# Performance work log

Hardware: AMD Instinct MI355X
Metric: run time of the kernel (lower is better)

The kernel has to match this reference:

```python
import jax, jax.numpy as jnp
import numpy as np

T, H, NH, NKV, HD, E, K, I = 1024, 2048, 16, 4, 128, 16, 2, 768
EPS = 1e-6
THETA = 10000.0


def setup_inputs() -> dict:
    key = jax.random.key(0)
    ks = jax.random.split(key, 8)
    s = 0.02
    return {
        "hidden_states": jax.random.normal(ks[0], (T, H), jnp.float32),
        "positions": jnp.arange(T, dtype=jnp.int32),
        "w_norm1": jnp.ones((H,), jnp.float32),
        "w_norm2": jnp.ones((H,), jnp.float32),
        "w_qkv": jax.random.normal(ks[1], (H, (NH + 2 * NKV) * HD), jnp.float32) * s,
        "w_qnorm": jnp.ones((HD,), jnp.float32),
        "w_knorm": jnp.ones((HD,), jnp.float32),
        "w_o": jax.random.normal(ks[2], (NH * HD, H), jnp.float32) * s,
        "w_router": jax.random.normal(ks[3], (H, E), jnp.float32) * s,
        "w_gate": jax.random.normal(ks[4], (E, H, I), jnp.float32) * s,
        "w_up": jax.random.normal(ks[5], (E, H, I), jnp.float32) * s,
        "w_down": jax.random.normal(ks[6], (E, I, H), jnp.float32) * s,
    }


def rmsnorm(x, w):
    return x * jax.lax.rsqrt(jnp.mean(x * x, axis=-1, keepdims=True) + EPS) * w


def apply_rope(x, positions):
    # NEOX-style rotary, full head_dim. x: [T, n_heads, HD]
    half = HD // 2
    inv_freq = 1.0 / (THETA ** (jnp.arange(half, dtype=jnp.float32) / half))
    ang = positions.astype(jnp.float32)[:, None] * inv_freq  # [T, half]
    cos = jnp.cos(ang)[:, None, :]
    sin = jnp.sin(ang)[:, None, :]
    x1, x2 = x[..., :half], x[..., half:]
    return jnp.concatenate([x1 * cos - x2 * sin, x2 * cos + x1 * sin], axis=-1)


def reference(hidden_states, positions, w_norm1, w_norm2, w_qkv, w_qnorm, w_knorm,
              w_o, w_router, w_gate, w_up, w_down):
    # prepare_attn: residual = x; h = input_layernorm(x)
    residual = hidden_states
    h = rmsnorm(hidden_states, w_norm1)

    # --- attention (bidirectional, GQA, per-head q/k RMSNorm + RoPE) ---
    qkv = h @ w_qkv
    q, k, v = jnp.split(qkv, [NH * HD, NH * HD + NKV * HD], axis=-1)
    q = rmsnorm(q.reshape(T, NH, HD), w_qnorm)
    k = rmsnorm(k.reshape(T, NKV, HD), w_knorm)
    v = v.reshape(T, NKV, HD)
    q = apply_rope(q, positions)
    k = apply_rope(k, positions)
    rep = NH // NKV
    kf = jnp.repeat(k, rep, axis=1)  # [T, NH, HD]
    vf = jnp.repeat(v, rep, axis=1)
    scores = jnp.einsum('tnd,snd->nts', q, kf) * (HD ** -0.5)  # [NH, T, T]
    p = jax.nn.softmax(scores, axis=-1)
    ctx = jnp.einsum('nts,snd->tnd', p, vf).reshape(T, NH * HD)
    attn_out = ctx @ w_o

    # prepare_mlp: residual = residual + attn_out; h = post_attention_layernorm(residual)
    residual = residual + attn_out
    h = rmsnorm(residual, w_norm2)

    # --- sparse MoE: softmax router, top-k renormalize, SwiGLU experts ---
    logits = h @ w_router
    probs = jax.nn.softmax(logits, axis=-1)
    topw, topi = jax.lax.top_k(probs, K)
    topw = topw / jnp.sum(topw, axis=-1, keepdims=True)
    gates = jnp.zeros((T, E), h.dtype).at[jnp.arange(T)[:, None], topi].set(topw)
    g = jnp.einsum('th,ehi->eti', h, w_gate)
    u = jnp.einsum('th,ehi->eti', h, w_up)
    y = jnp.einsum('eti,eih->eth', jax.nn.silu(g) * u, w_down)
    moe_out = jnp.einsum('eth,te->th', y, gates)

    return moe_out, residual
```

## Files before the change

### kernel.cpp

```cpp
#include <hip/hip_runtime.h>

#define T_    1024
#define H_    2048
#define NH_   16
#define NKV_  4
#define HD_   128
#define E_    16
#define I_    768
#define QKVN  3072

typedef __attribute__((ext_vector_type(8))) short  short8;
typedef __attribute__((ext_vector_type(4))) float  f32x4;
typedef unsigned short u16;

#define LDP 40

__device__ inline u16 f2bf(float f) {
  unsigned u = __builtin_bit_cast(unsigned, f);
  return (u16)((u + 0x7fffu + ((u >> 16) & 1u)) >> 16);
}
__device__ inline float bf2f(u16 h) {
  unsigned u = ((unsigned)h) << 16;
  return __builtin_bit_cast(float, u);
}

__device__ inline float blk_sum(float v, float* lds) {
#pragma unroll
  for (int o = 32; o; o >>= 1) v += __shfl_down(v, o);
  int w = threadIdx.x >> 6;
  __syncthreads();
  if ((threadIdx.x & 63) == 0) lds[w] = v;
  __syncthreads();
  float s = lds[0];
  int nw = blockDim.x >> 6;
  for (int i = 1; i < nw; ++i) s += lds[i];
  return s;
}
__device__ inline float blk_max(float v, float* lds) {
#pragma unroll
  for (int o = 32; o; o >>= 1) v = fmaxf(v, __shfl_down(v, o));
  int w = threadIdx.x >> 6;
  __syncthreads();
  if ((threadIdx.x & 63) == 0) lds[w] = v;
  __syncthreads();
  float s = lds[0];
  int nw = blockDim.x >> 6;
  for (int i = 1; i < nw; ++i) s = fmaxf(s, lds[i]);
  return s;
}


struct AU4 { uint4 v; };
struct BU2 { uint2 v; };
struct F4  { float v[4]; };

__device__ inline void wrS(u16* lds, const AU4& r) {
  *(uint4*)(lds + (threadIdx.x >> 2) * LDP + (threadIdx.x & 3) * 8) = r.v;
}
__device__ inline void wrS(u16* lds, const BU2& r) {
  *(uint2*)(lds + (threadIdx.x >> 3) * LDP + (threadIdx.x & 7) * 4) = r.v;
}
__device__ inline void wrS(u16* lds, const F4& r) {
  int n = threadIdx.x & 63, kh = (threadIdx.x >> 6) * 4;
  uint2 w;
  w.x = (unsigned)f2bf(r.v[0]) | ((unsigned)f2bf(r.v[1]) << 16);
  w.y = (unsigned)f2bf(r.v[2]) | ((unsigned)f2bf(r.v[3]) << 16);
  *(uint2*)(lds + n * LDP + kh) = w;
}

__device__ inline void mma2(const u16* As, const u16* Bs, f32x4 acc[2][2]) {
  const int lane = threadIdx.x & 63, wv = threadIdx.x >> 6;
  const int wr = wv >> 1, wc = wv & 1;
  const int kk = (lane >> 4) * 8, rr = lane & 15;
  short8 aF[2], bF[2];
#pragma unroll
  for (int m = 0; m < 2; ++m)
    aF[m] = *(const short8*)(As + (wr * 32 + m * 16 + rr) * LDP + kk);
#pragma unroll
  for (int n = 0; n < 2; ++n)
    bF[n] = *(const short8*)(Bs + (wc * 32 + n * 16 + rr) * LDP + kk);
#pragma unroll
  for (int m = 0; m < 2; ++m)
#pragma unroll
    for (int n = 0; n < 2; ++n)
      acc[m][n] = __builtin_amdgcn_mfma_f32_16x16x32_bf16(aF[m], bF[n], acc[m][n], 0, 0, 0);
}

#define ZERO_ACC(acc) do { \
  _Pragma("unroll") for (int m_ = 0; m_ < 2; ++m_) \
  _Pragma("unroll") for (int n_ = 0; n_ < 2; ++n_) acc[m_][n_] = (f32x4){0.f,0.f,0.f,0.f}; \
} while (0)

#define EPI_ROW(m, r)  (((threadIdx.x >> 6) >> 1) * 32 + (m)*16 + (((threadIdx.x&63) >> 4) * 4) + (r))
#define EPI_COL(n)     ((((threadIdx.x >> 6) & 1) * 32) + (n)*16 + ((threadIdx.x&63) & 15))

template<int NT, class AT, class BT, class LA, class LB>
__device__ inline void pipe2(LA la, LB lb, u16* A0, u16* B0, u16* A1, u16* B1,
                             f32x4 acc[2][2]) {
  AT a0, a1; BT b0, b1;
  la(a0, 0); lb(b0, 0);
  la(a1, 1); lb(b1, 1);
  wrS(A0, a0); wrS(B0, b0);
  if (NT > 2) { la(a0, 2); lb(b0, 2); }
#pragma unroll 1
  for (int kt = 0; kt < NT; kt += 2) {
    __syncthreads();
    wrS(A1, a1); wrS(B1, b1);
    if (kt + 3 < NT) { la(a1, kt + 3); lb(b1, kt + 3); }
    mma2(A0, B0, acc);
    __syncthreads();
    if (kt + 2 < NT) { wrS(A0, a0); wrS(B0, b0); }
    if (kt + 4 < NT) { la(a0, kt + 4); lb(b0, kt + 4); }
    mma2(A1, B1, acc);
  }
}


__global__ __launch_bounds__(256) void k_rms1(const float* x, const float* w, u16* out) {
  __shared__ float lds[4];
  int t = blockIdx.x, tid = threadIdx.x;
  float v[8]; float ss = 0.f;
#pragma unroll
  for (int i = 0; i < 8; ++i) { v[i] = x[(size_t)t * H_ + tid + 256 * i]; ss += v[i] * v[i]; }
  ss = blk_sum(ss, lds);
  float inv = rsqrtf(ss * (1.f / H_) + 1e-6f);
#pragma unroll
  for (int i = 0; i < 8; ++i)
    out[(size_t)t * H_ + tid + 256 * i] = f2bf(v[i] * inv * w[tid + 256 * i]);
}

__global__ __launch_bounds__(256) void k_rms2(const float* x, const float* w,
                                              float* outf, u16* outb) {
  __shared__ float lds[4];
  int t = blockIdx.x, tid = threadIdx.x;
  float v[8]; float ss = 0.f;
#pragma unroll
  for (int i = 0; i < 8; ++i) { v[i] = x[(size_t)t * H_ + tid + 256 * i]; ss += v[i] * v[i]; }
  ss = blk_sum(ss, lds);
  float inv = rsqrtf(ss * (1.f / H_) + 1e-6f);
#pragma unroll
  for (int i = 0; i < 8; ++i) {
    float r = v[i] * inv * w[tid + 256 * i];
    outf[(size_t)t * H_ + tid + 256 * i] = r;
    outb[(size_t)t * H_ + tid + 256 * i] = f2bf(r);
  }
}

__global__ __launch_bounds__(512) void k_qkv(const u16* h1, const float* wqkv, float* qkv) {
  __shared__ __align__(16) u16 A0[128 * LDP], B0[64 * LDP], A1[128 * LDP], B1[64 * LDP];
  int bn = blockIdx.x, bm = blockIdx.y;
  f32x4 acc[2][2]; ZERO_ACC(acc);
  auto la = [&](AU4& r, int kt) {
    r.v = *(const uint4*)(h1 + (size_t)(bm * 128 + (threadIdx.x >> 2)) * H_ + kt * 32 + (threadIdx.x & 3) * 8);
  };
  auto lb = [&](F4& r, int kt) {
    int n = threadIdx.x & 63, kh = (threadIdx.x >> 6) * 4;
    const float* src = wqkv + (size_t)(kt * 32 + kh) * QKVN + bn * 64 + n;
#pragma unroll
    for (int j = 0; j < 4; ++j) r.v[j] = src[(size_t)j * QKVN];
  };
  pipe2<H_ / 32, AU4, F4>(la, lb, A0, B0, A1, B1, acc);
#pragma unroll
  for (int m = 0; m < 2; ++m)
#pragma unroll
    for (int n = 0; n < 2; ++n) {
      f32x4 a = acc[m][n];
#pragma unroll
      for (int r = 0; r < 4; ++r)
        qkv[(size_t)(bm * 128 + EPI_ROW(m, r)) * QKVN + bn * 64 + EPI_COL(n)] = a[r];
    }
}

__global__ __launch_bounds__(256) void k_qkrope(const float* qkv, const int* pos,
                                                const float* wq, const float* wk,
                                                u16* q, u16* kk, u16* vT) {
  __shared__ float cs[64], sn[64];
  int t = blockIdx.x, tid = threadIdx.x, lane = tid & 63, w = tid >> 6;
  if (tid < 64) {
    float fr = expf(-((float)tid / 64.f) * 9.210340371976184f);
    float ang = (float)pos[t] * fr;
    float s_, c_; sincosf(ang, &s_, &c_);
    cs[tid] = c_; sn[tid] = s_;
  }
  __syncthreads();
  const float* row = qkv + (size_t)t * QKVN;
  for (int h = w; h < NH_; h += 4) {
    float x1 = row[h * 128 + lane], x2 = row[h * 128 + 64 + lane];
    float ss = x1 * x1 + x2 * x2;
#pragma unroll
    for (int o = 32; o; o >>= 1) ss += __shfl_down(ss, o);
    ss = __shfl(ss, 0);
    float inv = rsqrtf(ss * (1.f / HD_) + 1e-6f);
    float n1 = x1 * inv * wq[lane], n2 = x2 * inv * wq[64 + lane];
    float o1 = n1 * cs[lane] - n2 * sn[lane];
    float o2 = n2 * cs[lane] + n1 * sn[lane];
    q[(size_t)t * (NH_ * HD_) + h * 128 + lane] = f2bf(o1);
    q[(size_t)t * (NH_ * HD_) + h * 128 + 64 + lane] = f2bf(o2);
  }
  if (w < NKV_) {
    int h = w;
    float x1 = row[2048 + h * 128 + lane], x2 = row[2048 + h * 128 + 64 + lane];
    float ss = x1 * x1 + x2 * x2;
#pragma unroll
    for (int o = 32; o; o >>= 1) ss += __shfl_down(ss, o);
    ss = __shfl(ss, 0);
    float inv = rsqrtf(ss * (1.f / HD_) + 1e-6f);
    float n1 = x1 * inv * wk[lane], n2 = x2 * inv * wk[64 + lane];
    float o1 = n1 * cs[lane] - n2 * sn[lane];
    float o2 = n2 * cs[lane] + n1 * sn[lane];
    kk[((size_t)h * T_ + t) * HD_ + lane] = f2bf(o1);
    kk[((size_t)h * T_ + t) * HD_ + 64 + lane] = f2bf(o2);
    float v1 = row[2560 + h * 128 + lane], v2 = row[2560 + h * 128 + 64 + lane];
    vT[((size_t)(h * 128 + lane)) * T_ + t] = f2bf(v1);
    vT[((size_t)(h * 128 + 64 + lane)) * T_ + t] = f2bf(v2);
  }
}

__global__ __launch_bounds__(512) void k_scores(const u16* q, const u16* kb, u16* S) {
  __shared__ __align__(16) u16 A0[128 * LDP], B0[64 * LDP], A1[128 * LDP], B1[64 * LDP];
  int h = blockIdx.x, sn = blockIdx.y, qm = blockIdx.z;
  const u16* Aq = q + h * 128;
  const u16* Bk = kb + (size_t)(h >> 2) * T_ * HD_;
  f32x4 acc[2][2]; ZERO_ACC(acc);
  auto la = [&](AU4& r, int kt) {
    r.v = *(const uint4*)(Aq + (size_t)(qm * 128 + (threadIdx.x >> 2)) * (NH_ * HD_) + kt * 32 + (threadIdx.x & 3) * 8);
  };
  auto lb = [&](BU2& r, int kt) {
    r.v = *(const uint2*)(Bk + (size_t)(sn * 64 + (threadIdx.x >> 3)) * HD_ + kt * 32 + (threadIdx.x & 7) * 4);
  };
  pipe2<HD_ / 32, AU4, BU2>(la, lb, A0, B0, A1, B1, acc);
  const float scale = 0.08838834764831845f;
#pragma unroll
  for (int m = 0; m < 2; ++m)
#pragma unroll
    for (int n = 0; n < 2; ++n) {
      f32x4 a = acc[m][n];
#pragma unroll
      for (int r = 0; r < 4; ++r)
        S[((size_t)h * T_ + qm * 128 + EPI_ROW(m, r)) * T_ + sn * 64 + EPI_COL(n)] =
            f2bf(a[r] * scale);
    }
}

__global__ __launch_bounds__(256) void k_softmax(u16* S) {
  __shared__ float lds[4];
  int t = blockIdx.x, h = blockIdx.y, tid = threadIdx.x;
  u16* rowp = S + ((size_t)h * T_ + t) * T_;
  float x[4];
#pragma unroll
  for (int i = 0; i < 4; ++i) x[i] = bf2f(rowp[tid + 256 * i]);
  float m = fmaxf(fmaxf(x[0], x[1]), fmaxf(x[2], x[3]));
  m = blk_max(m, lds);
  float s = 0.f;
#pragma unroll
  for (int i = 0; i < 4; ++i) { x[i] = __expf(x[i] - m); s += x[i]; }
  s = blk_sum(s, lds);
  float inv = 1.f / s;
#pragma unroll
  for (int i = 0; i < 4; ++i) rowp[tid + 256 * i] = f2bf(x[i] * inv);
}

__global__ __launch_bounds__(512) void k_pv(const u16* P, const u16* vT, u16* ctx) {
  __shared__ __align__(16) u16 A0[128 * LDP], B0[64 * LDP], A1[128 * LDP], B1[64 * LDP];
  int h = blockIdx.x, qm = blockIdx.y, nb = blockIdx.z;
  const u16* Ap = P + (size_t)h * T_ * T_;
  const u16* Bv = vT + (size_t)(h >> 2) * HD_ * T_ + (size_t)nb * 64 * T_;
  f32x4 acc[2][2]; ZERO_ACC(acc);
  auto la = [&](AU4& r, int kt) {
    r.v = *(const uint4*)(Ap + (size_t)(qm * 128 + (threadIdx.x >> 2)) * T_ + kt * 32 + (threadIdx.x & 3) * 8);
  };
  auto lb = [&](BU2& r, int kt) {
    r.v = *(const uint2*)(Bv + (size_t)(threadIdx.x >> 3) * T_ + kt * 32 + (threadIdx.x & 7) * 4);
  };
  pipe2<T_ / 32, AU4, BU2>(la, lb, A0, B0, A1, B1, acc);
#pragma unroll
  for (int m = 0; m < 2; ++m)
#pragma unroll
    for (int n = 0; n < 2; ++n) {
      f32x4 a = acc[m][n];
#pragma unroll
      for (int r = 0; r < 4; ++r)
        ctx[(size_t)(qm * 128 + EPI_ROW(m, r)) * (NH_ * HD_) + h * 128 + nb * 64 + EPI_COL(n)] =
            f2bf(a[r]);
    }
}

__global__ __launch_bounds__(512) void k_wo(const u16* ctx, const float* wo,
                                            const float* hs, float* resid) {
  __shared__ __align__(16) u16 A0[128 * LDP], B0[64 * LDP], A1[128 * LDP], B1[64 * LDP];
  int bn = blockIdx.x, bm = blockIdx.y;
  f32x4 acc[2][2]; ZERO_ACC(acc);
  auto la = [&](AU4& r, int kt) {
    r.v = *(const uint4*)(ctx + (size_t)(bm * 128 + (threadIdx.x >> 2)) * H_ + kt * 32 + (threadIdx.x & 3) * 8);
  };
  auto lb = [&](F4& r, int kt) {
    int n = threadIdx.x & 63, kh = (threadIdx.x >> 6) * 4;
    const float* src = wo + (size_t)(kt * 32 + kh) * H_ + bn * 64 + n;
#pragma unroll
    for (int j = 0; j < 4; ++j) r.v[j] = src[(size_t)j * H_];
  };
  pipe2<H_ / 32, AU4, F4>(la, lb, A0, B0, A1, B1, acc);
#pragma unroll
  for (int m = 0; m < 2; ++m)
#pragma unroll
    for (int n = 0; n < 2; ++n) {
      f32x4 a = acc[m][n];
#pragma unroll
      for (int r = 0; r < 4; ++r) {
        size_t idx = (size_t)(bm * 128 + EPI_ROW(m, r)) * H_ + bn * 64 + EPI_COL(n);
        resid[idx] = a[r] + hs[idx];
      }
    }
}

__global__ __launch_bounds__(256) void k_router(const float* h2f, const float* wr_,
                                                int* topi, float* topw, int* cnt) {
  __shared__ float xs[H_];
  __shared__ float red[4][16];
  __shared__ float lg[16];
  int t = blockIdx.x, tid = threadIdx.x;
#pragma unroll
  for (int i = 0; i < 8; ++i) xs[tid + 256 * i] = h2f[(size_t)t * H_ + tid + 256 * i];
  __syncthreads();
  int e = tid & 15, p = tid >> 4;
  float s = 0.f;
  int b0 = p * 128;
  for (int i = 0; i < 128; ++i) s += xs[b0 + i] * wr_[(size_t)(b0 + i) * E_ + e];
  s += __shfl_down(s, 32);
  s += __shfl_down(s, 16);
  int lane = tid & 63, w = tid >> 6;
  if (lane < 16) red[w][lane] = s;
  __syncthreads();
  if (tid < 16) lg[tid] = red[0][tid] + red[1][tid] + red[2][tid] + red[3][tid];
  __syncthreads();
  if (tid == 0) {
    float l1 = -1e30f; int e1 = 0;
    for (int i = 0; i < E_; ++i) if (lg[i] > l1) { l1 = lg[i]; e1 = i; }
    float l2 = -1e30f; int e2 = 0;
    for (int i = 0; i < E_; ++i) if (i != e1 && lg[i] > l2) { l2 = lg[i]; e2 = i; }
    float d = __expf(l2 - l1);
    float w1 = 1.f / (1.f + d), w2 = d / (1.f + d);
    topi[2 * t] = e1; topi[2 * t + 1] = e2;
    topw[2 * t] = w1; topw[2 * t + 1] = w2;
    atomicAdd(&cnt[e1], 1);
    atomicAdd(&cnt[e2], 1);
  }
}

__global__ void k_scan(const int* cnt, int* basearr) {
  if (threadIdx.x == 0) {
    int b = 0;
    for (int e = 0; e < E_; ++e) { basearr[e] = b; b += cnt[e]; }
    basearr[E_] = b;
  }
}

__global__ __launch_bounds__(256) void k_assign(const int* topi, const float* topw,
                                                const int* basearr, int* posc,
                                                int* tok, float* wslot) {
  int t = blockIdx.x * 256 + threadIdx.x;
  if (t < T_) {
#pragma unroll
    for (int j = 0; j < 2; ++j) {
      int e = topi[2 * t + j];
      int p = atomicAdd(&posc[e], 1);
      int s = basearr[e] + p;
      tok[s] = t;
      wslot[s] = topw[2 * t + j];
    }
  }
}

__global__ __launch_bounds__(512) void k_gateup(const u16* h2b,
                                                const float* wg, const float* wu,
                                                const int* cnt, const int* basearr, const int* tok,
                                                u16* act) {
  __shared__ __align__(16) u16 A0[128 * LDP], B0[64 * LDP], A1[128 * LDP], B1[64 * LDP];
  __shared__ int gat_s[128];
  int e = blockIdx.x;
  int c = cnt[e];
  int mt = blockIdx.z;
  if (mt * 128 >= c) return;
  int basee = basearr[e];
  int gmax = c - mt * 128;
  int n0 = blockIdx.y * 32;
  int tid = threadIdx.x;
  if (tid < 128) {
    int r = mt * 128 + tid;
    gat_s[tid] = (r < c) ? tok[basee + r] : tok[basee];
  }
  __syncthreads();
  const float* Bg = wg + (size_t)e * H_ * I_;
  const float* Bu = wu + (size_t)e * H_ * I_;
  f32x4 acc[2][2]; ZERO_ACC(acc);
  auto la = [&](AU4& r, int kt) {
    r.v = *(const uint4*)(h2b + (size_t)gat_s[threadIdx.x >> 2] * H_ + kt * 32 + (threadIdx.x & 3) * 8);
  };
  auto lb = [&](F4& r, int kt) {
    int cidx = threadIdx.x & 63, kh = (threadIdx.x >> 6) * 4;
    int fn = cidx >> 4;
    const float* base = (fn & 1) ? Bu : Bg;
    int col = n0 + (fn >> 1) * 16 + (cidx & 15);
    const float* src = base + (size_t)(kt * 32 + kh) * I_ + col;
#pragma unroll
    for (int j = 0; j < 4; ++j) r.v[j] = src[(size_t)j * I_];
  };
  pipe2<H_ / 32, AU4, F4>(la, lb, A0, B0, A1, B1, acc);
  int slot0 = basee + mt * 128;
  int col = n0 + ((threadIdx.x >> 6) & 1) * 16 + ((threadIdx.x & 63) & 15);
#pragma unroll
  for (int m = 0; m < 2; ++m) {
#pragma unroll
    for (int r = 0; r < 4; ++r) {
      int row = EPI_ROW(m, r);
      if (row >= gmax) continue;
      float g = acc[m][0][r], u = acc[m][1][r];
      float sg = g / (1.f + __expf(-g));
      act[(size_t)(slot0 + row) * I_ + col] = f2bf(sg * u);
    }
  }
}

__global__ __launch_bounds__(512) void k_down(const u16* act, const float* wd,
                                              const int* cnt, const int* basearr,
                                              const int* tok, const float* wslot,
                                              float* moe) {
  __shared__ __align__(16) u16 A0[128 * LDP], B0[64 * LDP], A1[128 * LDP], B1[64 * LDP];
  int e = blockIdx.y;
  int c = cnt[e];
  int mt = blockIdx.z;
  if (mt * 128 >= c) return;
  int basee = basearr[e];
  int gmax = c - mt * 128;
  int slot0 = basee + mt * 128;
  int n0 = blockIdx.x * 64;
  const u16* Ap = act + (size_t)slot0 * I_;
  const float* Bp = wd + (size_t)e * I_ * H_;
  f32x4 acc[2][2]; ZERO_ACC(acc);
  auto la = [&](AU4& r, int kt) {
    r.v = *(const uint4*)(Ap + (size_t)(threadIdx.x >> 2) * I_ + kt * 32 + (threadIdx.x & 3) * 8);
  };
  auto lb = [&](F4& r, int kt) {
    int n = threadIdx.x & 63, kh = (threadIdx.x >> 6) * 4;
    const float* src = Bp + (size_t)(kt * 32 + kh) * H_ + n0 + n;
#pragma unroll
    for (int j = 0; j < 4; ++j) r.v[j] = src[(size_t)j * H_];
  };
  pipe2<I_ / 32, AU4, F4>(la, lb, A0, B0, A1, B1, acc);
#pragma unroll
  for (int m = 0; m < 2; ++m)
#pragma unroll
    for (int n = 0; n < 2; ++n) {
      f32x4 a = acc[m][n];
#pragma unroll
      for (int r = 0; r < 4; ++r) {
        int row = EPI_ROW(m, r);
        if (row >= gmax) continue;
        int col = EPI_COL(n);
        int slot = slot0 + row;
        float wgt = wslot[slot];
        int tk = tok[slot];
        atomicAdd(&moe[(size_t)tk * H_ + n0 + col], a[r] * wgt);
      }
    }
}

extern "C" void kernel_launch(void* const* d_in, const int* in_sizes, int n_in,
                              void* d_out, int out_size, void* d_ws, size_t ws_size,
                              hipStream_t stream) {
  const float* hs    = (const float*)d_in[0];
  const int*   pos   = (const int*)d_in[1];
  const float* wn1   = (const float*)d_in[2];
  const float* wn2   = (const float*)d_in[3];
  const float* wqkv  = (const float*)d_in[4];
  const float* wqn   = (const float*)d_in[5];
  const float* wkn   = (const float*)d_in[6];
  const float* wo    = (const float*)d_in[7];
  const float* wrt   = (const float*)d_in[8];
  const float* wg    = (const float*)d_in[9];
  const float* wu    = (const float*)d_in[10];
  const float* wd    = (const float*)d_in[11];
  float* out = (float*)d_out;
  float* moe_out = out;
  float* resid   = out + (size_t)T_ * H_;

  char* ws = (char*)d_ws;
  size_t off = 0;
  auto alloc = [&](size_t bytes) { size_t r = off; off = (off + bytes + 255) & ~(size_t)255; return r; };
  u16*   h1   = (u16*)  (ws + alloc((size_t)T_ * H_ * 2));
  float* qkv  = (float*)(ws + alloc((size_t)T_ * QKVN * 4));
  u16*   q    = (u16*)  (ws + alloc((size_t)T_ * NH_ * HD_ * 2));
  u16*   kb   = (u16*)  (ws + alloc((size_t)NKV_ * T_ * HD_ * 2));
  u16*   vT   = (u16*)  (ws + alloc((size_t)NKV_ * HD_ * T_ * 2));
  u16*   S    = (u16*)  (ws + alloc((size_t)NH_ * T_ * T_ * 2));
  u16*   ctx  = (u16*)  (ws + alloc((size_t)T_ * NH_ * HD_ * 2));
  float* h2f  = (float*)(ws + alloc((size_t)T_ * H_ * 4));
  u16*   h2b  = (u16*)  (ws + alloc((size_t)T_ * H_ * 2));
  u16*   act  = (u16*)  (ws + alloc((size_t)(2 * T_ + 256) * I_ * 2));
  int*   topi = (int*)  (ws + alloc((size_t)T_ * 2 * 4));
  float* topw = (float*)(ws + alloc((size_t)T_ * 2 * 4));
  int*   cnt  = (int*)  (ws + alloc(32 * 4));
  int*   posc = cnt + 16;
  int*   base = (int*)  (ws + alloc(32 * 4));
  int*   tok  = (int*)  (ws + alloc((size_t)(2 * T_ + 128) * 4));
  float* wsl  = (float*)(ws + alloc((size_t)(2 * T_ + 128) * 4));
  (void)ws_size; (void)in_sizes; (void)n_in; (void)out_size;

  hipMemsetAsync(moe_out, 0, (size_t)T_ * H_ * 4, stream);
  hipMemsetAsync(cnt, 0, 32 * 4, stream);

  k_rms1<<<T_, 256, 0, stream>>>(hs, wn1, h1);
  k_qkv<<<dim3(QKVN / 64, T_ / 128), 512, 0, stream>>>(h1, wqkv, qkv);
  k_qkrope<<<T_, 256, 0, stream>>>(qkv, pos, wqn, wkn, q, kb, vT);
  k_scores<<<dim3(NH_, T_ / 64, T_ / 128), 512, 0, stream>>>(q, kb, S);
  k_softmax<<<dim3(T_, NH_), 256, 0, stream>>>(S);
  k_pv<<<dim3(NH_, T_ / 128, HD_ / 64), 512, 0, stream>>>(S, vT, ctx);
  k_wo<<<dim3(H_ / 64, T_ / 128), 512, 0, stream>>>(ctx, wo, hs, resid);
  k_rms2<<<T_, 256, 0, stream>>>(resid, wn2, h2f, h2b);
  k_router<<<T_, 256, 0, stream>>>(h2f, wrt, topi, topw, cnt);
  k_scan<<<1, 64, 0, stream>>>(cnt, base);
  k_assign<<<4, 256, 0, stream>>>(topi, topw, base, posc, tok, wsl);
  k_gateup<<<dim3(E_, I_ / 32, T_ / 128), 512, 0, stream>>>(h2b, wg, wu, cnt, base, tok, act);
  k_down<<<dim3(H_ / 64, E_, T_ / 128), 512, 0, stream>>>(act, wd, cnt, base, tok, wsl, moe_out);
}
```

Measured before the change: 341.5 us.

## Load bf16 GEMM operands directly into LDS via global_load_lds

Replaces the register-staged loads of bf16 operand tiles (A everywhere, plus B in the scores and PV kernels) with the global_load_lds builtin, so data goes straight from global memory into shared memory. A tiles use an unpadded stride of 32 so they match the wave-contiguous layout the instruction writes. Two pipeline variants are added: one for bf16 A with fp32 B still converted in registers, and one fully direct for bf16×bf16. This removes VGPR staging and LDS store instructions, but the unpadded A layout may cause LDS bank conflicts on MFMA fragment reads. The direct loads also depend on __syncthreads being enough to order them, with no explicit vmcnt wait.

```diff
diff --git a/kernel.cpp b/kernel.cpp
--- a/kernel.cpp
+++ b/kernel.cpp
@@ -13,7 +13,8 @@
 typedef __attribute__((ext_vector_type(4))) float  f32x4;
 typedef unsigned short u16;
 
-#define LDP 40
+#define LDPA 32
+#define LDPB 40
 
 __device__ inline u16 f2bf(float f) {
   unsigned u = __builtin_bit_cast(unsigned, f);
@@ -22,6 +23,12 @@
 __device__ inline float bf2f(u16 h) {
   unsigned u = ((unsigned)h) << 16;
   return __builtin_bit_cast(float, u);
+}
+
+__device__ inline void gll16(const u16* g, u16* l) {
+  __builtin_amdgcn_global_load_lds(
+      (const __attribute__((address_space(1))) void*)g,
+      (__attribute__((address_space(3))) void*)l, 16, 0, 0);
 }
 
 __device__ inline float blk_sum(float v, float* lds) {
@@ -50,24 +57,17 @@
 }
 
 
-struct AU4 { uint4 v; };
-struct BU2 { uint2 v; };
-struct F4  { float v[4]; };
-
-__device__ inline void wrS(u16* lds, const AU4& r) {
-  *(uint4*)(lds + (threadIdx.x >> 2) * LDP + (threadIdx.x & 3) * 8) = r.v;
-}
-__device__ inline void wrS(u16* lds, const BU2& r) {
-  *(uint2*)(lds + (threadIdx.x >> 3) * LDP + (threadIdx.x & 7) * 4) = r.v;
-}
+struct F4 { float v[4]; };
+
 __device__ inline void wrS(u16* lds, const F4& r) {
   int n = threadIdx.x & 63, kh = (threadIdx.x >> 6) * 4;
   uint2 w;
   w.x = (unsigned)f2bf(r.v[0]) | ((unsigned)f2bf(r.v[1]) << 16);
   w.y = (unsigned)f2bf(r.v[2]) | ((unsigned)f2bf(r.v[3]) << 16);
-  *(uint2*)(lds + n * LDP + kh) = w;
-}
-
+  *(uint2*)(lds + n * LDPB + kh) = w;
+}
+
+template<int SA, int SB>
 __device__ inline void mma2(const u16* As, const u16* Bs, f32x4 acc[2][2]) {
   const int lane = threadIdx.x & 63, wv = threadIdx.x >> 6;
   const int wr = wv >> 1, wc = wv & 1;
@@ -75,10 +75,10 @@
   short8 aF[2], bF[2];
 #pragma unroll
   for (int m = 0; m < 2; ++m)
-    aF[m] = *(const short8*)(As + (wr * 32 + m * 16 + rr) * LDP + kk);
+    aF[m] = *(const short8*)(As + (wr * 32 + m * 16 + rr) * SA + kk);
 #pragma unroll
   for (int n = 0; n < 2; ++n)
-    bF[n] = *(const short8*)(Bs + (wc * 32 + n * 16 + rr) * LDP + kk);
+    bF[n] = *(const short8*)(Bs + (wc * 32 + n * 16 + rr) * SB + kk);
 #pragma unroll
   for (int m = 0; m < 2; ++m)
 #pragma unroll
@@ -94,24 +94,40 @@
 #define EPI_ROW(m, r)  (((threadIdx.x >> 6) >> 1) * 32 + (m)*16 + (((threadIdx.x&63) >> 4) * 4) + (r))
 #define EPI_COL(n)     ((((threadIdx.x >> 6) & 1) * 32) + (n)*16 + ((threadIdx.x&63) & 15))
 
-template<int NT, class AT, class BT, class LA, class LB>
-__device__ inline void pipe2(LA la, LB lb, u16* A0, u16* B0, u16* A1, u16* B1,
-                             f32x4 acc[2][2]) {
-  AT a0, a1; BT b0, b1;
-  la(a0, 0); lb(b0, 0);
-  la(a1, 1); lb(b1, 1);
-  wrS(A0, a0); wrS(B0, b0);
-  if (NT > 2) { la(a0, 2); lb(b0, 2); }
+template<int NT, class GA, class LB>
+__device__ inline void pipeGF(GA ga, LB lb, u16* A0, u16* B0, u16* A1, u16* B1,
+                              f32x4 acc[2][2]) {
+  F4 b0, b1;
+  ga(A0, 0);
+  lb(b0, 0); lb(b1, 1);
+  wrS(B0, b0);
+  if (NT > 2) lb(b0, 2);
 #pragma unroll 1
   for (int kt = 0; kt < NT; kt += 2) {
     __syncthreads();
-    wrS(A1, a1); wrS(B1, b1);
-    if (kt + 3 < NT) { la(a1, kt + 3); lb(b1, kt + 3); }
-    mma2(A0, B0, acc);
+    ga(A1, kt + 1);
+    wrS(B1, b1);
+    if (kt + 3 < NT) lb(b1, kt + 3);
+    mma2<LDPA, LDPB>(A0, B0, acc);
     __syncthreads();
-    if (kt + 2 < NT) { wrS(A0, a0); wrS(B0, b0); }
-    if (kt + 4 < NT) { la(a0, kt + 4); lb(b0, kt + 4); }
-    mma2(A1, B1, acc);
+    if (kt + 2 < NT) { ga(A0, kt + 2); wrS(B0, b0); }
+    if (kt + 4 < NT) lb(b0, kt + 4);
+    mma2<LDPA, LDPB>(A1, B1, acc);
+  }
+}
+
+template<int NT, class GA, class GB>
+__device__ inline void pipeGG(GA ga, GB gb, u16* A0, u16* B0, u16* A1, u16* B1,
+                              f32x4 acc[2][2]) {
+  ga(A0, 0); gb(B0, 0);
+#pragma unroll 1
+  for (int kt = 0; kt < NT; kt += 2) {
+    __syncthreads();
+    ga(A1, kt + 1); gb(B1, kt + 1);
+    mma2<LDPA, LDPA>(A0, B0, acc);
+    __syncthreads();
+    if (kt + 2 < NT) { ga(A0, kt + 2); gb(B0, kt + 2); }
+    mma2<LDPA, LDPA>(A1, B1, acc);
   }
 }
 
@@ -147,11 +163,13 @@
 }
 
 __global__ __launch_bounds__(512) void k_qkv(const u16* h1, const float* wqkv, float* qkv) {
-  __shared__ __align__(16) u16 A0[128 * LDP], B0[64 * LDP], A1[128 * LDP], B1[64 * LDP];
+  __shared__ __align__(16) u16 A0[128 * LDPA], A1[128 * LDPA];
+  __shared__ __align__(16) u16 B0[64 * LDPB], B1[64 * LDPB];
   int bn = blockIdx.x, bm = blockIdx.y;
   f32x4 acc[2][2]; ZERO_ACC(acc);
-  auto la = [&](AU4& r, int kt) {
-    r.v = *(const uint4*)(h1 + (size_t)(bm * 128 + (threadIdx.x >> 2)) * H_ + kt * 32 + (threadIdx.x & 3) * 8);
+  auto ga = [&](u16* As, int kt) {
+    gll16(h1 + (size_t)(bm * 128 + (threadIdx.x >> 2)) * H_ + kt * 32 + (threadIdx.x & 3) * 8,
+          As + (threadIdx.x & 448) * 8);
   };
   auto lb = [&](F4& r, int kt) {
     int n = threadIdx.x & 63, kh = (threadIdx.x >> 6) * 4;
@@ -159,7 +177,7 @@
 #pragma unroll
     for (int j = 0; j < 4; ++j) r.v[j] = src[(size_t)j * QKVN];
   };
-  pipe2<H_ / 32, AU4, F4>(la, lb, A0, B0, A1, B1, acc);
+  pipeGF<H_ / 32>(ga, lb, A0, B0, A1, B1, acc);
 #pragma unroll
   for (int m = 0; m < 2; ++m)
 #pragma unroll
@@ -217,18 +235,22 @@
 }
 
 __global__ __launch_bounds__(512) void k_scores(const u16* q, const u16* kb, u16* S) {
-  __shared__ __align__(16) u16 A0[128 * LDP], B0[64 * LDP], A1[128 * LDP], B1[64 * LDP];
+  __shared__ __align__(16) u16 A0[128 * LDPA], A1[128 * LDPA];
+  __shared__ __align__(16) u16 B0[64 * LDPA], B1[64 * LDPA];
   int h = blockIdx.x, sn = blockIdx.y, qm = blockIdx.z;
   const u16* Aq = q + h * 128;
   const u16* Bk = kb + (size_t)(h >> 2) * T_ * HD_;
   f32x4 acc[2][2]; ZERO_ACC(acc);
-  auto la = [&](AU4& r, int kt) {
-    r.v = *(const uint4*)(Aq + (size_t)(qm * 128 + (threadIdx.x >> 2)) * (NH_ * HD_) + kt * 32 + (threadIdx.x & 3) * 8);
-  };
-  auto lb = [&](BU2& r, int kt) {
-    r.v = *(const uint2*)(Bk + (size_t)(sn * 64 + (threadIdx.x >> 3)) * HD_ + kt * 32 + (threadIdx.x & 7) * 4);
-  };
-  pipe2<HD_ / 32, AU4, BU2>(la, lb, A0, B0, A1, B1, acc);
+  auto ga = [&](u16* As, int kt) {
+    gll16(Aq + (size_t)(qm * 128 + (threadIdx.x >> 2)) * (NH_ * HD_) + kt * 32 + (threadIdx.x & 3) * 8,
+          As + (threadIdx.x & 448) * 8);
+  };
+  auto gb = [&](u16* Bs, int kt) {
+    if (threadIdx.x < 256)
+      gll16(Bk + (size_t)(sn * 64 + (threadIdx.x >> 2)) * HD_ + kt * 32 + (threadIdx.x & 3) * 8,
+            Bs + (threadIdx.x & 192) * 8);
+  };
+  pipeGG<HD_ / 32>(ga, gb, A0, B0, A1, B1, acc);
   const float scale = 0.08838834764831845f;
 #pragma unroll
   for (int m = 0; m < 2; ++m)
@@ -261,18 +283,22 @@
 }
 
 __global__ __launch_bounds__(512) void k_pv(const u16* P, const u16* vT, u16* ctx) {
-  __shared__ __align__(16) u16 A0[128 * LDP], B0[64 * LDP], A1[128 * LDP], B1[64 * LDP];
+  __shared__ __align__(16) u16 A0[128 * LDPA], A1[128 * LDPA];
+  __shared__ __align__(16) u16 B0[64 * LDPA], B1[64 * LDPA];
   int h = blockIdx.x, qm = blockIdx.y, nb = blockIdx.z;
   const u16* Ap = P + (size_t)h * T_ * T_;
   const u16* Bv = vT + (size_t)(h >> 2) * HD_ * T_ + (size_t)nb * 64 * T_;
   f32x4 acc[2][2]; ZERO_ACC(acc);
-  auto la = [&](AU4& r, int kt) {
-    r.v = *(const uint4*)(Ap + (size_t)(qm * 128 + (threadIdx.x >> 2)) * T_ + kt * 32 + (threadIdx.x & 3) * 8);
-  };
-  auto lb = [&](BU2& r, int kt) {
-    r.v = *(const uint2*)(Bv + (size_t)(threadIdx.x >> 3) * T_ + kt * 32 + (threadIdx.x & 7) * 4);
-  };
-  pipe2<T_ / 32, AU4, BU2>(la, lb, A0, B0, A1, B1, acc);
+  auto ga = [&](u16* As, int kt) {
+    gll16(Ap + (size_t)(qm * 128 + (threadIdx.x >> 2)) * T_ + kt * 32 + (threadIdx.x & 3) * 8,
+          As + (threadIdx.x & 448) * 8);
+  };
+  auto gb = [&](u16* Bs, int kt) {
+    if (threadIdx.x < 256)
+      gll16(Bv + (size_t)(threadIdx.x >> 2) * T_ + kt * 32 + (threadIdx.x & 3) * 8,
+            Bs + (threadIdx.x & 192) * 8);
+  };
+  pipeGG<T_ / 32>(ga, gb, A0, B0, A1, B1, acc);
 #pragma unroll
   for (int m = 0; m < 2; ++m)
 #pragma unroll
@@ -287,11 +313,13 @@
 
 __global__ __launch_bounds__(512) void k_wo(const u16* ctx, const float* wo,
                                             const float* hs, float* resid) {
-  __shared__ __align__(16) u16 A0[128 * LDP], B0[64 * LDP], A1[128 * LDP], B1[64 * LDP];
+  __shared__ __align__(16) u16 A0[128 * LDPA], A1[128 * LDPA];
+  __shared__ __align__(16) u16 B0[64 * LDPB], B1[64 * LDPB];
   int bn = blockIdx.x, bm = blockIdx.y;
   f32x4 acc[2][2]; ZERO_ACC(acc);
-  auto la = [&](AU4& r, int kt) {
-    r.v = *(const uint4*)(ctx + (size_t)(bm * 128 + (threadIdx.x >> 2)) * H_ + kt * 32 + (threadIdx.x & 3) * 8);
+  auto ga = [&](u16* As, int kt) {
+    gll16(ctx + (size_t)(bm * 128 + (threadIdx.x >> 2)) * H_ + kt * 32 + (threadIdx.x & 3) * 8,
+          As + (threadIdx.x & 448) * 8);
   };
   auto lb = [&](F4& r, int kt) {
     int n = threadIdx.x & 63, kh = (threadIdx.x >> 6) * 4;
@@ -299,7 +327,7 @@
 #pragma unroll
     for (int j = 0; j < 4; ++j) r.v[j] = src[(size_t)j * H_];
   };
-  pipe2<H_ / 32, AU4, F4>(la, lb, A0, B0, A1, B1, acc);
+  pipeGF<H_ / 32>(ga, lb, A0, B0, A1, B1, acc);
 #pragma unroll
   for (int m = 0; m < 2; ++m)
 #pragma unroll
@@ -375,7 +403,8 @@
                                                 const float* wg, const float* wu,
                                                 const int* cnt, const int* basearr, const int* tok,
                                                 u16* act) {
-  __shared__ __align__(16) u16 A0[128 * LDP], B0[64 * LDP], A1[128 * LDP], B1[64 * LDP];
+  __shared__ __align__(16) u16 A0[128 * LDPA], A1[128 * LDPA];
+  __shared__ __align__(16) u16 B0[64 * LDPB], B1[64 * LDPB];
   __shared__ int gat_s[128];
   int e = blockIdx.x;
   int c = cnt[e];
@@ -390,14 +419,15 @@
     gat_s[tid] = (r < c) ? tok[basee + r] : tok[basee];
   }
   __syncthreads();
+  int grow = gat_s[tid >> 2];
   const float* Bg = wg + (size_t)e * H_ * I_;
   const float* Bu = wu + (size_t)e * H_ * I_;
   f32x4 acc[2][2]; ZERO_ACC(acc);
-  auto la = [&](AU4& r, int kt) {
-    r.v = *(const uint4*)(h2b + (size_t)gat_s[threadIdx.x >> 2] * H_ + kt * 32 + (threadIdx.x & 3) * 8);
+  auto ga = [&](u16* As, int kt) {
+    gll16(h2b + (size_t)grow * H_ + kt * 32 + (tid & 3) * 8, As + (tid & 448) * 8);
   };
   auto lb = [&](F4& r, int kt) {
-    int cidx = threadIdx.x & 63, kh = (threadIdx.x >> 6) * 4;
+    int cidx = tid & 63, kh = (tid >> 6) * 4;
     int fn = cidx >> 4;
     const float* base = (fn & 1) ? Bu : Bg;
     int col = n0 + (fn >> 1) * 16 + (cidx & 15);
@@ -405,9 +435,9 @@
 #pragma unroll
     for (int j = 0; j < 4; ++j) r.v[j] = src[(size_t)j * I_];
   };
-  pipe2<H_ / 32, AU4, F4>(la, lb, A0, B0, A1, B1, acc);
+  pipeGF<H_ / 32>(ga, lb, A0, B0, A1, B1, acc);
   int slot0 = basee + mt * 128;
-  int col = n0 + ((threadIdx.x >> 6) & 1) * 16 + ((threadIdx.x & 63) & 15);
+  int col = n0 + ((tid >> 6) & 1) * 16 + ((tid & 63) & 15);
 #pragma unroll
   for (int m = 0; m < 2; ++m) {
 #pragma unroll
@@ -425,7 +455,8 @@
                                               const int* cnt, const int* basearr,
                                               const int* tok, const float* wslot,
                                               float* moe) {
-  __shared__ __align__(16) u16 A0[128 * LDP], B0[64 * LDP], A1[128 * LDP], B1[64 * LDP];
+  __shared__ __align__(16) u16 A0[128 * LDPA], A1[128 * LDPA];
+  __shared__ __align__(16) u16 B0[64 * LDPB], B1[64 * LDPB];
   int e = blockIdx.y;
   int c = cnt[e];
   int mt = blockIdx.z;
@@ -437,8 +468,9 @@
   const u16* Ap = act + (size_t)slot0 * I_;
   const float* Bp = wd + (size_t)e * I_ * H_;
   f32x4 acc[2][2]; ZERO_ACC(acc);
-  auto la = [&](AU4& r, int kt) {
-    r.v = *(const uint4*)(Ap + (size_t)(threadIdx.x >> 2) * I_ + kt * 32 + (threadIdx.x & 3) * 8);
+  auto ga = [&](u16* As, int kt) {
+    gll16(Ap + (size_t)(threadIdx.x >> 2) * I_ + kt * 32 + (threadIdx.x & 3) * 8,
+          As + (threadIdx.x & 448) * 8);
   };
   auto lb = [&](F4& r, int kt) {
     int n = threadIdx.x & 63, kh = (threadIdx.x >> 6) * 4;
@@ -446,7 +478,7 @@
 #pragma unroll
     for (int j = 0; j < 4; ++j) r.v[j] = src[(size_t)j * H_];
   };
-  pipe2<I_ / 32, AU4, F4>(la, lb, A0, B0, A1, B1, acc);
+  pipeGF<I_ / 32>(ga, lb, A0, B0, A1, B1, acc);
 #pragma unroll
   for (int m = 0; m < 2; ++m)
 #pragma unroll
```

Result: faster. 331.9 us (-2.8%).
